# Kernel tuning notes

Hardware: AMD Instinct MI355X
Metric: run time of the kernel (lower is better)

## Reference

```python
import jax, jax.numpy as jnp
import numpy as np

K = 3          # kernel size
PAD = 1
K2 = K * K
G = 4          # groups (conv groups == offset groups)
EPS = 1e-5


def _conv2d(x, w, b):
    # x: [N,C,H,W], w: [O,I,kh,kw], stride 1, pad 1
    y = jax.lax.conv_general_dilated(
        x, w, window_strides=(1, 1), padding=((PAD, PAD), (PAD, PAD)),
        dimension_numbers=("NCHW", "OIHW", "NCHW"))
    return y + b[None, :, None, None]


def _deform_conv(x2d, offset, conv_w, conv_b):
    # x2d: [N,C,H,W]; offset: [N, 2*G*K2, H, W] (layout: 2*(g*K2+k)+{0:y,1:x})
    N, C, H, W = x2d.shape
    Cg = C // G
    Cout = conv_w.shape[0]
    Og = Cout // G

    off = offset.reshape(N, G, K2, 2, H, W)
    off_y = off[:, :, :, 0]          # [N,G,K2,H,W]
    off_x = off[:, :, :, 1]

    kk = jnp.arange(K, dtype=offset.dtype) - PAD            # [-1,0,1]
    ky2 = jnp.repeat(kk, K)                                  # k = kh*K + kw
    kx2 = jnp.tile(kk, K)
    base_y = jnp.arange(H, dtype=offset.dtype)[None, :] + ky2[:, None]  # [K2,H]
    base_x = jnp.arange(W, dtype=offset.dtype)[None, :] + kx2[:, None]  # [K2,W]

    py = off_y + base_y[None, None, :, :, None]   # [N,G,K2,H,W]
    px = off_x + base_x[None, None, :, None, :]

    y0f = jnp.floor(py); x0f = jnp.floor(px)
    ly = py - y0f; lx = px - x0f
    y0 = y0f.astype(jnp.int32); x0 = x0f.astype(jnp.int32)
    y1 = y0 + 1; x1 = x0 + 1

    # channels-last grouped view for gathers: [N,G,H,W,Cg]
    xg = x2d.reshape(N, G, Cg, H, W).transpose(0, 1, 3, 4, 2)
    nI = jnp.arange(N)[:, None, None, None, None]
    gI = jnp.arange(G)[None, :, None, None, None]

    def corner(yi, xi):
        valid = (yi >= 0) & (yi < H) & (xi >= 0) & (xi < W)
        yc = jnp.clip(yi, 0, H - 1)
        xc = jnp.clip(xi, 0, W - 1)
        v = xg[nI, gI, yc, xc]                    # [N,G,K2,H,W,Cg]
        return v * valid[..., None].astype(x2d.dtype)

    w00 = ((1 - ly) * (1 - lx))[..., None]
    w01 = ((1 - ly) * lx)[..., None]
    w10 = (ly * (1 - lx))[..., None]
    w11 = (ly * lx)[..., None]
    sampled = (w00 * corner(y0, x0) + w01 * corner(y0, x1)
               + w10 * corner(y1, x0) + w11 * corner(y1, x1))  # [N,G,K2,H,W,Cg]

    wG = conv_w.reshape(G, Og, Cg, K2)
    out = jnp.einsum('ngkhwc,gock->ngohw', sampled, wG)         # [N,G,Og,H,W]
    out = out.reshape(N, Cout, H, W) + conv_b[None, :, None, None]
    return out


def setup_inputs() -> dict:
    key = jax.random.key(0)
    ks = jax.random.split(key, 5)
    B, C, D, H, W = 2, 128, 6, 56, 56
    Cout = 128
    x = jax.random.normal(ks[0], (B, C, D, H, W), dtype=jnp.float32)
    # offset conv: small init so sampling displacements stay modest
    offset_w = jax.random.normal(ks[1], (2 * G * K2, C, K, K), dtype=jnp.float32) * 0.01
    offset_b = jnp.zeros((2 * G * K2,), dtype=jnp.float32)
    fan_in = (C // G) * K2
    conv_w = jax.random.normal(ks[2], (Cout, C // G, K, K), dtype=jnp.float32) / np.sqrt(fan_in)
    conv_b = jax.random.normal(ks[3], (Cout,), dtype=jnp.float32) * 0.01
    return {"x": x, "offset_w": offset_w, "offset_b": offset_b,
            "conv_w": conv_w, "conv_b": conv_b}


def reference(x, offset_w, offset_b, conv_w, conv_b):
    B, C, D, H, W = x.shape
    x2d = x.transpose(0, 2, 1, 3, 4).reshape(B * D, C, H, W)
    offset = _conv2d(x2d, offset_w, offset_b)
    out = _deform_conv(x2d, offset, conv_w, conv_b)           # [B*D, Cout, H, W]
    Cout = out.shape[1]
    out = out.reshape(B, D, Cout, H, W).transpose(0, 2, 1, 3, 4)  # [B,Cout,D,H,W]
    # instance norm: per (b, c) over (D, H, W), no affine
    mu = jnp.mean(out, axis=(2, 3, 4), keepdims=True)
    var = jnp.var(out, axis=(2, 3, 4), keepdims=True)
    out = (out - mu) * jax.lax.rsqrt(var + EPS)
    # exact GELU
    return 0.5 * out * (1.0 + jax.lax.erf(out / jnp.sqrt(2.0).astype(out.dtype)))
```

## Files before the change

### kernel.cpp

```cpp
#include <hip/hip_runtime.h>
#include <hip/hip_bf16.h>

typedef __attribute__((ext_vector_type(8))) short bf16x8;
typedef __attribute__((ext_vector_type(4))) float f32x4;

#define B_   2
#define C_   128
#define D_   6
#define H_   56
#define W_   56
#define N_   12
#define HW   3136
#define CSTR (D_*HW)
#define COUT 128
#define OFFP 80

__device__ __forceinline__ float bf2f(ushort u) {
  return __uint_as_float(((unsigned int)u) << 16);
}
__device__ __forceinline__ ushort f2bf(float f) {
  unsigned int x = __float_as_uint(f);
  x += 0x7FFFu + ((x >> 16) & 1u);
  return (ushort)(x >> 16);
}

__global__ __launch_bounds__(256) void k_transpose(const float* __restrict__ x,
                                                   ushort* __restrict__ xcl) {
  __shared__ float tile[32][57];
  const int h = blockIdx.x, c0 = blockIdx.y * 32, n = blockIdx.z;
  const int b = n / D_, d = n % D_;
  const float* src = x + (((size_t)(b * C_ + c0) * D_ + d) * HW) + h * W_;
  for (int i = threadIdx.x; i < 32 * W_; i += 256) {
    const int c = i / W_, w = i - c * W_;
    tile[c][w] = src[(size_t)c * CSTR + w];
  }
  __syncthreads();
  ushort* dst = xcl + ((size_t)(n * HW + h * W_)) * C_ + c0;
  for (int i = threadIdx.x; i < 32 * W_; i += 256) {
    const int w = i >> 5, c = i & 31;
    dst[(size_t)w * C_ + c] = f2bf(tile[c][w]);
  }
}

__global__ void k_wdef2(const float* __restrict__ cw, ushort* __restrict__ wd2) {
  const int idx = blockIdx.x * 256 + threadIdx.x;
  if (idx < COUT * 288) {
    const int g = idx / 9216;
    const int r = idx - g * 9216;
    const int kb = r >> 8;
    const int co_l = (r >> 3) & 31;
    const int e = r & 7;
    const int ts = kb >> 2;
    const int q = kb & 3;
    wd2[idx] = f2bf(cw[((size_t)(g * 32 + co_l) * 32 + q * 8 + e) * 9 + ts]);
  }
}

__global__ void k_woff2(const float* __restrict__ ow, ushort* __restrict__ wob2) {
  const int idx = blockIdx.x * 256 + threadIdx.x;
  if (idx < 144 * OFFP * 8) {
    const int e = idx & 7;
    const int co = (idx >> 3) % OFFP;
    const int kb = idx / (OFFP * 8);
    const int tap = kb >> 4;
    const int r16 = kb & 15;
    const int kq = r16 >> 2;
    const int q = r16 & 3;
    const int c = kq * 32 + q * 8 + e;
    float v = 0.f;
    if (co < 72) v = ow[((size_t)co * C_ + c) * 9 + tap];
    wob2[idx] = f2bf(v);
  }
}

__global__ __launch_bounds__(320) void k_offset_conv(const ushort* __restrict__ xcl,
    const ushort* __restrict__ wob2, const float* __restrict__ ob,
    float* __restrict__ offb2) {
  __shared__ __align__(16) ushort xr[3 * 24 * 128];
  const int w0 = blockIdx.x * 16;
  const int h = blockIdx.y, n = blockIdx.z;
  const int t = threadIdx.x;
  for (int i = t; i < 864; i += 320) {
    const int c16 = i & 15;
    const int sdy = i >> 4;
    const int s = sdy % 18;
    const int dy = sdy / 18;
    const int w = w0 - 1 + s;
    const int rr = h + dy - 1;
    const int c0 = c16 * 8;
    const int db = (((dy * 24 + s) * 128 + c0) * 2) ^ ((s & 7) << 4);
    uint4 v = {0u, 0u, 0u, 0u};
    if ((unsigned)rr < (unsigned)H_ && (unsigned)w < (unsigned)W_)
      v = *(const uint4*)(xcl + ((size_t)(n * HW + rr * W_ + w)) * C_ + c0);
    *(uint4*)((char*)xr + db) = v;
  }
  __syncthreads();
  const int l = t & 63;
  const int nt = t >> 6;
  const int lf = l & 15, q = l >> 4;
  f32x4 acc = {};
#pragma unroll 3
  for (int tap = 0; tap < 9; ++tap) {
    const int dy = tap / 3, kxr = tap - dy * 3;
    const int s = lf + kxr;
#pragma unroll
    for (int kq = 0; kq < 4; ++kq) {
      const int ab = (((dy * 24 + s) * 128 + kq * 32 + q * 8) * 2) ^ ((s & 7) << 4);
      const bf16x8 a = *(const bf16x8*)((const char*)xr + ab);
      const bf16x8 bb = *(const bf16x8*)(wob2 +
          ((size_t)(tap * 16 + kq * 4 + q) * OFFP + nt * 16 + lf) * 8);
      acc = __builtin_amdgcn_mfma_f32_16x16x32_bf16(a, bb, acc, 0, 0, 0);
    }
  }
  const int co = nt * 16 + lf;
  const float bias = (co < 72) ? ob[co] : 0.f;
  float* orow = offb2 + ((size_t)n * HW + h * W_) * OFFP;
#pragma unroll
  for (int r = 0; r < 4; ++r) {
    const int w = w0 + q * 4 + r;
    if (w < W_) orow[(size_t)w * OFFP + co] = acc[r] + bias;
  }
}

__global__ __launch_bounds__(256) void k_deform(const ushort* __restrict__ xcl,
    const float* __restrict__ offb2, const ushort* __restrict__ wd2,
    const float* __restrict__ cb, float* __restrict__ out) {
  __shared__ __align__(16) ushort ss[16 * 1160];
  __shared__ __align__(16) unsigned char sm2[14080];
  ushort* swW = (ushort*)sm2;
  int* swO = (int*)(sm2 + 4608);
  float* outs = (float*)sm2;

  const int hw0 = blockIdx.x * 16;
  const int n = blockIdx.y;
  const int t = threadIdx.x;

  for (int i = t; i < 576; i += 256) {
    const int p = i / 36;
    const int r = i - p * 36;
    const int g = r / 9;
    const int k = r - g * 9;
    const int hw = hw0 + p;
    const int h = hw / 56;
    const int w = hw - h * 56;
    const float2 o2 = *(const float2*)(offb2 + (size_t)(n * HW + hw) * OFFP + g * 18 + 2 * k);
    const int ky = k / 3 - 1;
    const int kx = k - (k / 3) * 3 - 1;
    const float py = (float)(h + ky) + o2.x;
    const float px = (float)(w + kx) + o2.y;
    const float y0f = floorf(py), x0f = floorf(px);
    const float ly = py - y0f, lx = px - x0f;
    const int y0 = (int)y0f, x0 = (int)x0f;
    const int y1 = y0 + 1, x1 = x0 + 1;
    const int yc0 = min(max(y0, 0), H_ - 1), yc1 = min(max(y1, 0), H_ - 1);
    const int xc0 = min(max(x0, 0), W_ - 1), xc1 = min(max(x1, 0), W_ - 1);
    const float my0 = ((unsigned)y0 < (unsigned)H_) ? 1.f : 0.f;
    const float my1 = ((unsigned)y1 < (unsigned)H_) ? 1.f : 0.f;
    const float mx0 = ((unsigned)x0 < (unsigned)W_) ? 1.f : 0.f;
    const float mx1 = ((unsigned)x1 < (unsigned)W_) ? 1.f : 0.f;
    ushort4 wq;
    wq.x = f2bf((1.f - ly) * (1.f - lx) * my0 * mx0);
    wq.y = f2bf((1.f - ly) * lx * my0 * mx1);
    wq.z = f2bf(ly * (1.f - lx) * my1 * mx0);
    wq.w = f2bf(ly * lx * my1 * mx1);
    *(ushort4*)(swW + p * 144 + (g * 9 + k) * 4) = wq;
    const int gb = g * 32;
    int4 oq;
    oq.x = (yc0 * 56 + xc0) * 128 + gb;
    oq.y = (yc0 * 56 + xc1) * 128 + gb;
    oq.z = (yc1 * 56 + xc0) * 128 + gb;
    oq.w = (yc1 * 56 + xc1) * 128 + gb;
    *(int4*)(swO + p * 148 + (g * 9 + k) * 4) = oq;
  }
  __syncthreads();

  {
    const int c4 = t & 7;
    const int p = (t >> 3) & 15;
    const int gh = t >> 7;
    const ushort* xb = xcl + (size_t)n * HW * C_ + c4 * 4;
#pragma unroll
    for (int gg = 0; gg < 2; ++gg) {
      const int g = gh * 2 + gg;
      ushort* sd = ss + p * 1160 + g * 288 + c4 * 4;
      const int wb = p * 144 + g * 36;
      const int obi = p * 148 + g * 36;
#pragma unroll 3
      for (int k = 0; k < 9; ++k) {
        const ushort4 wq = *(const ushort4*)(swW + wb + k * 4);
        const int4 oq = *(const int4*)(swO + obi + k * 4);
        const ushort4 a0 = *(const ushort4*)(xb + oq.x);
        const ushort4 a1 = *(const ushort4*)(xb + oq.y);
        const ushort4 a2 = *(const ushort4*)(xb + oq.z);
        const ushort4 a3 = *(const ushort4*)(xb + oq.w);
        const float w00 = bf2f(wq.x), w01 = bf2f(wq.y);
        const float w10 = bf2f(wq.z), w11 = bf2f(wq.w);
        ushort4 rr;
        rr.x = f2bf(fmaf(w00, bf2f(a0.x), fmaf(w01, bf2f(a1.x), fmaf(w10, bf2f(a2.x), w11 * bf2f(a3.x)))));
        rr.y = f2bf(fmaf(w00, bf2f(a0.y), fmaf(w01, bf2f(a1.y), fmaf(w10, bf2f(a2.y), w11 * bf2f(a3.y)))));
        rr.z = f2bf(fmaf(w00, bf2f(a0.z), fmaf(w01, bf2f(a1.z), fmaf(w10, bf2f(a2.z), w11 * bf2f(a3.z)))));
        rr.w = f2bf(fmaf(w00, bf2f(a0.w), fmaf(w01, bf2f(a1.w), fmaf(w10, bf2f(a2.w), w11 * bf2f(a3.w)))));
        *(ushort4*)(sd + k * 32) = rr;
      }
    }
  }
  __syncthreads();

  const int l = t & 63;
  const int g = t >> 6;
  const int lf = l & 15, q = l >> 4;
  f32x4 acc0 = {}, acc1 = {};
  {
    const ushort* arow = ss + lf * 1160 + g * 288 + q * 8;
    const ushort* bb = wd2 + (size_t)g * 36 * 32 * 8 + (size_t)q * 32 * 8 + lf * 8;
#pragma unroll
    for (int ts = 0; ts < 9; ++ts) {
      const bf16x8 a = *(const bf16x8*)(arow + ts * 32);
      const bf16x8 b0 = *(const bf16x8*)(bb + ts * 4 * 32 * 8);
      const bf16x8 b1 = *(const bf16x8*)(bb + ts * 4 * 32 * 8 + 16 * 8);
      acc0 = __builtin_amdgcn_mfma_f32_16x16x32_bf16(a, b0, acc0, 0, 0, 0);
      acc1 = __builtin_amdgcn_mfma_f32_16x16x32_bf16(a, b1, acc1, 0, 0, 0);
    }
  }
#pragma unroll
  for (int r = 0; r < 4; ++r) {
    outs[(g * 32 + lf) * 20 + q * 4 + r] = acc0[r] + cb[g * 32 + lf];
    outs[(g * 32 + 16 + lf) * 20 + q * 4 + r] = acc1[r] + cb[g * 32 + 16 + lf];
  }
  __syncthreads();
  {
    const int co = t & 127;
    const int hf = t >> 7;
    const float4 v0 = *(const float4*)(outs + co * 20 + hf * 8);
    const float4 v1 = *(const float4*)(outs + co * 20 + hf * 8 + 4);
    const int b = n / D_, d = n - b * D_;
    float* dst = out + ((size_t)(b * COUT + co) * D_ + d) * HW + hw0 + hf * 8;
    *(float4*)dst = v0;
    *(float4*)(dst + 4) = v1;
  }
}

__global__ __launch_bounds__(512) void k_norm_gelu(float* __restrict__ io) {
  const int M = D_ * HW;
  const int M4 = M / 4;
  float4* p = (float4*)(io + (size_t)blockIdx.x * M);
  float s = 0.f, s2 = 0.f;
  for (int i = threadIdx.x; i < M4; i += 512) {
    const float4 v = p[i];
    s += v.x + v.y + v.z + v.w;
    s2 = fmaf(v.x, v.x, fmaf(v.y, v.y, fmaf(v.z, v.z, fmaf(v.w, v.w, s2))));
  }
#pragma unroll
  for (int off = 32; off > 0; off >>= 1) {
    s += __shfl_down(s, off, 64);
    s2 += __shfl_down(s2, off, 64);
  }
  __shared__ float rs[8], rs2[8];
  __shared__ float smu, srstd;
  const int wid = threadIdx.x >> 6, lane = threadIdx.x & 63;
  if (lane == 0) { rs[wid] = s; rs2[wid] = s2; }
  __syncthreads();
  if (threadIdx.x == 0) {
    float ts = 0.f, t2 = 0.f;
#pragma unroll
    for (int i = 0; i < 8; ++i) { ts += rs[i]; t2 += rs2[i]; }
    const float mu = ts / (float)M;
    const float var = t2 / (float)M - mu * mu;
    smu = mu;
    srstd = rsqrtf(var + 1e-5f);
  }
  __syncthreads();
  const float mu = smu, rstd = srstd;
  for (int i = threadIdx.x; i < M4; i += 512) {
    float4 v = p[i];
    v.x = (v.x - mu) * rstd; v.y = (v.y - mu) * rstd;
    v.z = (v.z - mu) * rstd; v.w = (v.w - mu) * rstd;
    v.x = 0.5f * v.x * (1.f + erff(v.x * 0.70710678118654752f));
    v.y = 0.5f * v.y * (1.f + erff(v.y * 0.70710678118654752f));
    v.z = 0.5f * v.z * (1.f + erff(v.z * 0.70710678118654752f));
    v.w = 0.5f * v.w * (1.f + erff(v.w * 0.70710678118654752f));
    p[i] = v;
  }
}

extern "C" void kernel_launch(void* const* d_in, const int* in_sizes, int n_in,
                              void* d_out, int out_size, void* d_ws, size_t ws_size,
                              hipStream_t stream) {
  const float* x  = (const float*)d_in[0];
  const float* ow = (const float*)d_in[1];
  const float* ob = (const float*)d_in[2];
  const float* cw = (const float*)d_in[3];
  const float* cb = (const float*)d_in[4];
  float* outp = (float*)d_out;

  char* wsb = (char*)d_ws;
  ushort* xcl   = (ushort*)wsb;
  float*  offb2 = (float*)(wsb + 9633792);
  ushort* wd2   = (ushort*)(wsb + 21676032);
  ushort* wob2  = (ushort*)(wsb + 21749760);

  k_wdef2<<<dim3(144), 256, 0, stream>>>(cw, wd2);
  k_woff2<<<dim3(360), 256, 0, stream>>>(ow, wob2);
  k_transpose<<<dim3(H_, 4, N_), 256, 0, stream>>>(x, xcl);
  k_offset_conv<<<dim3(4, H_, N_), 320, 0, stream>>>(xcl, wob2, ob, offb2);
  k_deform<<<dim3(196, N_), 256, 0, stream>>>(xcl, offb2, wd2, cb, outp);
  k_norm_gelu<<<dim3(B_ * COUT), 512, 0, stream>>>(outp);
}
```

Measured before the change: 169.5 us.

## Fuse bilinear sampling into MFMA operand build and merge weight-prep kernels

Result: no change. 171.8 us (+1.4%).

```diff
diff --git a/kernel.cpp b/kernel.cpp
--- a/kernel.cpp
+++ b/kernel.cpp
@@ -42,7 +42,8 @@
   }
 }
 
-__global__ void k_wdef2(const float* __restrict__ cw, ushort* __restrict__ wd2) {
+__global__ void k_wprep(const float* __restrict__ cw, const float* __restrict__ ow,
+                        ushort* __restrict__ wd2, ushort* __restrict__ wob2) {
   const int idx = blockIdx.x * 256 + threadIdx.x;
   if (idx < COUT * 288) {
     const int g = idx / 9216;
@@ -53,15 +54,11 @@
     const int ts = kb >> 2;
     const int q = kb & 3;
     wd2[idx] = f2bf(cw[((size_t)(g * 32 + co_l) * 32 + q * 8 + e) * 9 + ts]);
-  }
-}
-
-__global__ void k_woff2(const float* __restrict__ ow, ushort* __restrict__ wob2) {
-  const int idx = blockIdx.x * 256 + threadIdx.x;
-  if (idx < 144 * OFFP * 8) {
-    const int e = idx & 7;
-    const int co = (idx >> 3) % OFFP;
-    const int kb = idx / (OFFP * 8);
+  } else if (idx < COUT * 288 + 144 * OFFP * 8) {
+    const int i2 = idx - COUT * 288;
+    const int e = i2 & 7;
+    const int co = (i2 >> 3) % OFFP;
+    const int kb = i2 / (OFFP * 8);
     const int tap = kb >> 4;
     const int r16 = kb & 15;
     const int kq = r16 >> 2;
@@ -69,7 +66,7 @@
     const int c = kq * 32 + q * 8 + e;
     float v = 0.f;
     if (co < 72) v = ow[((size_t)co * C_ + c) * 9 + tap];
-    wob2[idx] = f2bf(v);
+    wob2[i2] = f2bf(v);
   }
 }
 
@@ -125,11 +122,10 @@
 __global__ __launch_bounds__(256) void k_deform(const ushort* __restrict__ xcl,
     const float* __restrict__ offb2, const ushort* __restrict__ wd2,
     const float* __restrict__ cb, float* __restrict__ out) {
-  __shared__ __align__(16) ushort ss[16 * 1160];
-  __shared__ __align__(16) unsigned char sm2[14080];
-  ushort* swW = (ushort*)sm2;
-  int* swO = (int*)(sm2 + 4608);
-  float* outs = (float*)sm2;
+  __shared__ __align__(16) unsigned char sm[14208];
+  __shared__ __align__(16) float outs[2560];
+  ushort* swW = (ushort*)sm;
+  int* swO = (int*)(sm + 4736);
 
   const int hw0 = blockIdx.x * 16;
   const int n = blockIdx.y;
@@ -163,64 +159,55 @@
     wq.y = f2bf((1.f - ly) * lx * my0 * mx1);
     wq.z = f2bf(ly * (1.f - lx) * my1 * mx0);
     wq.w = f2bf(ly * lx * my1 * mx1);
-    *(ushort4*)(swW + p * 144 + (g * 9 + k) * 4) = wq;
-    const int gb = g * 32;
+    *(ushort4*)(swW + p * 148 + (g * 9 + k) * 4) = wq;
     int4 oq;
-    oq.x = (yc0 * 56 + xc0) * 128 + gb;
-    oq.y = (yc0 * 56 + xc1) * 128 + gb;
-    oq.z = (yc1 * 56 + xc0) * 128 + gb;
-    oq.w = (yc1 * 56 + xc1) * 128 + gb;
+    oq.x = (yc0 * 56 + xc0) * 128;
+    oq.y = (yc0 * 56 + xc1) * 128;
+    oq.z = (yc1 * 56 + xc0) * 128;
+    oq.w = (yc1 * 56 + xc1) * 128;
     *(int4*)(swO + p * 148 + (g * 9 + k) * 4) = oq;
-  }
-  __syncthreads();
-
-  {
-    const int c4 = t & 7;
-    const int p = (t >> 3) & 15;
-    const int gh = t >> 7;
-    const ushort* xb = xcl + (size_t)n * HW * C_ + c4 * 4;
-#pragma unroll
-    for (int gg = 0; gg < 2; ++gg) {
-      const int g = gh * 2 + gg;
-      ushort* sd = ss + p * 1160 + g * 288 + c4 * 4;
-      const int wb = p * 144 + g * 36;
-      const int obi = p * 148 + g * 36;
-#pragma unroll 3
-      for (int k = 0; k < 9; ++k) {
-        const ushort4 wq = *(const ushort4*)(swW + wb + k * 4);
-        const int4 oq = *(const int4*)(swO + obi + k * 4);
-        const ushort4 a0 = *(const ushort4*)(xb + oq.x);
-        const ushort4 a1 = *(const ushort4*)(xb + oq.y);
-        const ushort4 a2 = *(const ushort4*)(xb + oq.z);
-        const ushort4 a3 = *(const ushort4*)(xb + oq.w);
-        const float w00 = bf2f(wq.x), w01 = bf2f(wq.y);
-        const float w10 = bf2f(wq.z), w11 = bf2f(wq.w);
-        ushort4 rr;
-        rr.x = f2bf(fmaf(w00, bf2f(a0.x), fmaf(w01, bf2f(a1.x), fmaf(w10, bf2f(a2.x), w11 * bf2f(a3.x)))));
-        rr.y = f2bf(fmaf(w00, bf2f(a0.y), fmaf(w01, bf2f(a1.y), fmaf(w10, bf2f(a2.y), w11 * bf2f(a3.y)))));
-        rr.z = f2bf(fmaf(w00, bf2f(a0.z), fmaf(w01, bf2f(a1.z), fmaf(w10, bf2f(a2.z), w11 * bf2f(a3.z)))));
-        rr.w = f2bf(fmaf(w00, bf2f(a0.w), fmaf(w01, bf2f(a1.w), fmaf(w10, bf2f(a2.w), w11 * bf2f(a3.w)))));
-        *(ushort4*)(sd + k * 32) = rr;
-      }
-    }
   }
   __syncthreads();
 
   const int l = t & 63;
   const int g = t >> 6;
   const int lf = l & 15, q = l >> 4;
+  const ushort* xb = xcl + (size_t)n * HW * C_ + g * 32 + q * 8;
+  const ushort* bb = wd2 + ((size_t)(g * 36 + q) * 32 + lf) * 8;
+  const int sbase = lf * 148 + g * 36;
   f32x4 acc0 = {}, acc1 = {};
-  {
-    const ushort* arow = ss + lf * 1160 + g * 288 + q * 8;
-    const ushort* bb = wd2 + (size_t)g * 36 * 32 * 8 + (size_t)q * 32 * 8 + lf * 8;
-#pragma unroll
-    for (int ts = 0; ts < 9; ++ts) {
-      const bf16x8 a = *(const bf16x8*)(arow + ts * 32);
-      const bf16x8 b0 = *(const bf16x8*)(bb + ts * 4 * 32 * 8);
-      const bf16x8 b1 = *(const bf16x8*)(bb + ts * 4 * 32 * 8 + 16 * 8);
-      acc0 = __builtin_amdgcn_mfma_f32_16x16x32_bf16(a, b0, acc0, 0, 0, 0);
-      acc1 = __builtin_amdgcn_mfma_f32_16x16x32_bf16(a, b1, acc1, 0, 0, 0);
+#pragma unroll 3
+  for (int ts = 0; ts < 9; ++ts) {
+    const ushort4 wq = *(const ushort4*)(swW + sbase + ts * 4);
+    const int4 oq = *(const int4*)(swO + sbase + ts * 4);
+    const uint4 c00 = *(const uint4*)(xb + oq.x);
+    const uint4 c01 = *(const uint4*)(xb + oq.y);
+    const uint4 c10 = *(const uint4*)(xb + oq.z);
+    const uint4 c11 = *(const uint4*)(xb + oq.w);
+    const float w00 = bf2f(wq.x), w01 = bf2f(wq.y);
+    const float w10 = bf2f(wq.z), w11 = bf2f(wq.w);
+    bf16x8 av;
+#pragma unroll
+    for (int j = 0; j < 4; ++j) {
+      const unsigned int u00 = ((const unsigned int*)&c00)[j];
+      const unsigned int u01 = ((const unsigned int*)&c01)[j];
+      const unsigned int u10 = ((const unsigned int*)&c10)[j];
+      const unsigned int u11 = ((const unsigned int*)&c11)[j];
+      const float lo = fmaf(w00, __uint_as_float(u00 << 16),
+                       fmaf(w01, __uint_as_float(u01 << 16),
+                       fmaf(w10, __uint_as_float(u10 << 16),
+                            w11 * __uint_as_float(u11 << 16))));
+      const float hi = fmaf(w00, __uint_as_float(u00 & 0xFFFF0000u),
+                       fmaf(w01, __uint_as_float(u01 & 0xFFFF0000u),
+                       fmaf(w10, __uint_as_float(u10 & 0xFFFF0000u),
+                            w11 * __uint_as_float(u11 & 0xFFFF0000u))));
+      av[2 * j]     = (short)f2bf(lo);
+      av[2 * j + 1] = (short)f2bf(hi);
     }
+    const bf16x8 b0 = *(const bf16x8*)(bb + (size_t)ts * 4 * 32 * 8);
+    const bf16x8 b1 = *(const bf16x8*)(bb + (size_t)ts * 4 * 32 * 8 + 16 * 8);
+    acc0 = __builtin_amdgcn_mfma_f32_16x16x32_bf16(av, b0, acc0, 0, 0, 0);
+    acc1 = __builtin_amdgcn_mfma_f32_16x16x32_bf16(av, b1, acc1, 0, 0, 0);
   }
 #pragma unroll
   for (int r = 0; r < 4; ++r) {
@@ -299,8 +286,7 @@
   ushort* wd2   = (ushort*)(wsb + 21676032);
   ushort* wob2  = (ushort*)(wsb + 21749760);
 
-  k_wdef2<<<dim3(144), 256, 0, stream>>>(cw, wd2);
-  k_woff2<<<dim3(360), 256, 0, stream>>>(ow, wob2);
+  k_wprep<<<dim3(504), 256, 0, stream>>>(cw, ow, wd2, wob2);
   k_transpose<<<dim3(H_, 4, N_), 256, 0, stream>>>(x, xcl);
   k_offset_conv<<<dim3(4, H_, N_), 320, 0, stream>>>(xcl, wob2, ob, offb2);
   k_deform<<<dim3(196, N_), 256, 0, stream>>>(xcl, offb2, wd2, cb, outp);
```
